# Kernel tuning notes

Hardware: AMD Instinct MI355X
Metric: run time of the kernel (lower is better)

The kernel has to match this reference:

```python
import jax, jax.numpy as jnp
import numpy as np

N_NODES = 50000
N_EDGES = 600000
NODE_DIM = 64
EDGE_DIM = 16
HIDDEN = 128
N_LAYERS = 3
N_CLASSES = 2
N_GRAPHS = 256
BN_EPS = 1e-5


def setup_inputs() -> dict:
    key = jax.random.key(0)
    ks = jax.random.split(key, 24)
    i = iter(range(24))
    def nrm(shape, scale=0.05):
        return jax.random.normal(ks[next(i)], shape, dtype=jnp.float32) * scale
    inp = {
        "x": jax.random.normal(ks[next(i)], (N_NODES, NODE_DIM), dtype=jnp.float32),
        "edge_index": jax.random.randint(ks[next(i)], (2, N_EDGES), 0, N_NODES),
        "edge_attr": jax.random.normal(ks[next(i)], (N_EDGES, EDGE_DIM), dtype=jnp.float32),
        "batch": jnp.sort(jax.random.randint(ks[next(i)], (N_NODES,), 0, N_GRAPHS)),
        # encoders
        "node_w": nrm((NODE_DIM, HIDDEN)), "node_b": jnp.zeros((HIDDEN,), jnp.float32),
        "edge_w": nrm((EDGE_DIM, HIDDEN)), "edge_b": jnp.zeros((HIDDEN,), jnp.float32),
        # per-layer GINE MLP params, stacked over layers
        "mlp_w1": nrm((N_LAYERS, HIDDEN, HIDDEN)), "mlp_b1": jnp.zeros((N_LAYERS, HIDDEN), jnp.float32),
        "mlp_w2": nrm((N_LAYERS, HIDDEN, HIDDEN)), "mlp_b2": jnp.zeros((N_LAYERS, HIDDEN), jnp.float32),
        "bn_gamma": jnp.ones((N_LAYERS, HIDDEN), jnp.float32), "bn_beta": jnp.zeros((N_LAYERS, HIDDEN), jnp.float32),
        # head
        "head_w1": nrm((HIDDEN, HIDDEN)), "head_b1": jnp.zeros((HIDDEN,), jnp.float32),
        "head_w2": nrm((HIDDEN, N_CLASSES)), "head_b2": jnp.zeros((N_CLASSES,), jnp.float32),
    }
    return inp


def _forward(x, edge_attr, node_w, node_b, edge_w, edge_b, mlp_w1, mlp_b1,
             mlp_w2, mlp_b2, bn_gamma, bn_beta, head_w1, head_b1, head_w2,
             head_b2, edge_index, batch):
    src, dst = edge_index[0], edge_index[1]
    h = x @ node_w + node_b                     # [N, H]
    ea = edge_attr @ edge_w + edge_b            # [E, H]
    for l in range(N_LAYERS):
        # GINE message: relu(x_src + edge_attr), scatter-add into dst
        msg = jax.nn.relu(h[src] + ea)          # [E, H]
        agg = jax.ops.segment_sum(msg, dst, num_segments=N_NODES)
        z = h + agg                              # (1+eps)*x + agg, eps=0
        z = jax.nn.relu(z @ mlp_w1[l] + mlp_b1[l]) @ mlp_w2[l] + mlp_b2[l]
        # BatchNorm1d over node dim (batch statistics)
        mean = jnp.mean(z, axis=0)
        var = jnp.var(z, axis=0)
        z = bn_gamma[l] * (z - mean) * jax.lax.rsqrt(var + BN_EPS) + bn_beta[l]
        h = jax.nn.relu(z)                       # dropout off (eval)
    g = jax.ops.segment_sum(h, batch, num_segments=N_GRAPHS)  # global_add_pool
    return jax.nn.relu(g @ head_w1 + head_b1) @ head_w2 + head_b2


def reference(x, edge_index, edge_attr, batch, node_w, node_b, edge_w, edge_b,
              mlp_w1, mlp_b1, mlp_w2, mlp_b2, bn_gamma, bn_beta,
              head_w1, head_b1, head_w2, head_b2):
    return _forward(x, edge_attr, node_w, node_b, edge_w, edge_b, mlp_w1,
                    mlp_b1, mlp_w2, mlp_b2, bn_gamma, bn_beta, head_w1,
                    head_b1, head_w2, head_b2, edge_index, batch)
```

## Files before the change

### kernel.cpp

```cpp
#include <hip/hip_runtime.h>

#define N_NODES_C 50000
#define N_EDGES_C 600000
#define NODE_DIM_C 64
#define EDGE_DIM_C 16
#define HID 128
#define N_GRAPHS_C 256
#define BN_EPS_C 1e-5f
#define SCAN_NBLK ((N_NODES_C + 255) / 256)

typedef short bf16x8 __attribute__((ext_vector_type(8)));
typedef float f32x4 __attribute__((ext_vector_type(4)));
typedef float f32x2 __attribute__((ext_vector_type(2)));

__device__ __forceinline__ unsigned short f2bf(float f) {
  union { float f; unsigned u; } v; v.f = f;
  unsigned r = (v.u + 0x7fffu + ((v.u >> 16) & 1u)) >> 16;
  return (unsigned short)r;
}

__device__ __forceinline__ float2 bfp2f(unsigned u) {
  union { unsigned u; float f; } lo, hi;
  lo.u = u << 16;
  hi.u = u & 0xffff0000u;
  return make_float2(lo.f, hi.f);
}

__device__ __forceinline__ float bf2f(unsigned short s) {
  union { unsigned u; float f; } v;
  v.u = ((unsigned)s) << 16;
  return v.f;
}

__device__ __forceinline__ float2 fp8p2f(unsigned short u) {
  f32x2 r = __builtin_amdgcn_cvt_pk_f32_fp8((int)(unsigned)u, false);
  return make_float2(r.x, r.y);
}

__global__ __launch_bounds__(256)
void k_x2bf(const float* __restrict__ x, unsigned short* __restrict__ xb,
            int* __restrict__ cnt, float* __restrict__ g) {
  int tid = blockIdx.x * 256 + threadIdx.x;
  size_t i = (size_t)tid * 4;
  if (i < (size_t)N_NODES_C * NODE_DIM_C) {
    float4 v = *(const float4*)&x[i];
    uint2 o;
    o.x = (unsigned)f2bf(v.x) | ((unsigned)f2bf(v.y) << 16);
    o.y = (unsigned)f2bf(v.z) | ((unsigned)f2bf(v.w) << 16);
    *(uint2*)&xb[i] = o;
  }
  if (tid < N_NODES_C) cnt[tid] = 0;
  if (tid < N_GRAPHS_C * HID) g[tid] = 0.f;
}

__global__ __launch_bounds__(256)
void k_prep_w(const float* __restrict__ w1, const float* __restrict__ w2,
              const float* __restrict__ nodew, unsigned short* __restrict__ wT) {
  int m = blockIdx.x;
  if (m < 6) {
    const float* src = (m < 3) ? (w1 + (size_t)m * HID * HID)
                               : (w2 + (size_t)(m - 3) * HID * HID);
    unsigned short* dst = wT + (size_t)m * HID * HID;
    for (int i = threadIdx.x; i < HID * HID; i += 256) {
      int n = i >> 7, k = i & 127;
      dst[n * HID + k] = f2bf(src[k * HID + n]);
    }
  } else {
    unsigned short* dst = wT + (size_t)6 * HID * HID;
    for (int i = threadIdx.x; i < HID * NODE_DIM_C; i += 256) {
      int n = i >> 6, k = i & 63;
      dst[n * NODE_DIM_C + k] = f2bf(nodew[k * HID + n]);
    }
  }
}

__global__ __launch_bounds__(256)
void k_node_mfma(const unsigned short* __restrict__ xb,
                 const unsigned short* __restrict__ nwT,
                 const float* __restrict__ bias, unsigned short* __restrict__ h) {
  const int LD = NODE_DIM_C + 8;
  __shared__ unsigned short a_lds[128 * LD];
  __shared__ unsigned short w_lds[128 * LD];
  int t = threadIdx.x;
  int row0 = blockIdx.x * 128;
  {
    int r = t >> 3, c = t & 7;
#pragma unroll
    for (int it = 0; it < 4; ++it) {
      int row = it * 32 + r;
      int grow = row0 + row;
      uint4 va = (grow < N_NODES_C)
                     ? ((const uint4*)(xb + (size_t)grow * NODE_DIM_C))[c]
                     : make_uint4(0, 0, 0, 0);
      *(uint4*)&a_lds[row * LD + c * 8] = va;
      uint4 vw = ((const uint4*)(nwT + (size_t)row * NODE_DIM_C))[c];
      *(uint4*)&w_lds[row * LD + c * 8] = vw;
    }
  }
  __syncthreads();

  int lane = t & 63;
  int w = t >> 6;
  int l15 = lane & 15;
  int q = lane >> 4;

  f32x4 acc[2][8];
#pragma unroll
  for (int rt = 0; rt < 2; ++rt)
#pragma unroll
    for (int nt = 0; nt < 8; ++nt) acc[rt][nt] = (f32x4)0.f;

#pragma unroll
  for (int kk = 0; kk < 2; ++kk) {
    int k0 = kk * 32;
    bf16x8 af[2];
#pragma unroll
    for (int rt = 0; rt < 2; ++rt) {
      int arow = w * 32 + rt * 16 + l15;
      af[rt] = *(const bf16x8*)&a_lds[arow * LD + k0 + q * 8];
    }
#pragma unroll
    for (int nt = 0; nt < 8; ++nt) {
      bf16x8 bf = *(const bf16x8*)&w_lds[(nt * 16 + l15) * LD + k0 + q * 8];
#pragma unroll
      for (int rt = 0; rt < 2; ++rt)
        acc[rt][nt] = __builtin_amdgcn_mfma_f32_16x16x32_bf16(af[rt], bf, acc[rt][nt], 0, 0, 0);
    }
  }

#pragma unroll
  for (int nt = 0; nt < 8; ++nt) {
    int gcol = nt * 16 + l15;
    float bv = bias[gcol];
#pragma unroll
    for (int rt = 0; rt < 2; ++rt) {
#pragma unroll
      for (int i = 0; i < 4; ++i) {
        int grow = row0 + w * 32 + rt * 16 + q * 4 + i;
        if (grow < N_NODES_C) h[(size_t)grow * HID + gcol] = f2bf(acc[rt][nt][i] + bv);
      }
    }
  }
}

__global__ __launch_bounds__(256)
void k_histogram(const int* __restrict__ dst, int* __restrict__ counts) {
  int e = blockIdx.x * 256 + threadIdx.x;
  if (e < N_EDGES_C) atomicAdd(&counts[dst[e]], 1);
}

__global__ __launch_bounds__(256)
void k_blocksum(const int* __restrict__ cnt, int* __restrict__ partial) {
  __shared__ int ls[4];
  int t = threadIdx.x;
  int i = blockIdx.x * 256 + t;
  int v = (i < N_NODES_C) ? cnt[i] : 0;
#pragma unroll
  for (int o = 32; o > 0; o >>= 1) v += __shfl_down(v, o, 64);
  if ((t & 63) == 0) ls[t >> 6] = v;
  __syncthreads();
  if (t == 0) partial[blockIdx.x] = ls[0] + ls[1] + ls[2] + ls[3];
}

__global__ __launch_bounds__(256)
void k_scanpartials(const int* __restrict__ partial, int* __restrict__ partial_off) {
  __shared__ int s[256];
  int t = threadIdx.x;
  int v = (t < SCAN_NBLK) ? partial[t] : 0;
  s[t] = v;
  __syncthreads();
  for (int d = 1; d < 256; d <<= 1) {
    int x = (t >= d) ? s[t - d] : 0;
    __syncthreads();
    s[t] += x;
    __syncthreads();
  }
  if (t < SCAN_NBLK) partial_off[t] = s[t] - v;
}

__global__ __launch_bounds__(256)
void k_apply(int* __restrict__ cnt_cursor, const int* __restrict__ partial_off,
             int* __restrict__ row_ptr) {
  __shared__ int s[256];
  int t = threadIdx.x;
  int i = blockIdx.x * 256 + t;
  int v = (i < N_NODES_C) ? cnt_cursor[i] : 0;
  s[t] = v;
  __syncthreads();
  for (int d = 1; d < 256; d <<= 1) {
    int x = (t >= d) ? s[t - d] : 0;
    __syncthreads();
    s[t] += x;
    __syncthreads();
  }
  int excl = s[t] - v + partial_off[blockIdx.x];
  if (i < N_NODES_C) {
    row_ptr[i] = excl;
    cnt_cursor[i] = excl;
  }
  if (i == 0) row_ptr[N_NODES_C] = N_EDGES_C;
}

__global__ __launch_bounds__(256)
void k_bucket(const int* __restrict__ dst, const int* __restrict__ srcArr,
              int* __restrict__ cursor, int* __restrict__ perm,
              int* __restrict__ src_perm) {
  int e = blockIdx.x * 256 + threadIdx.x;
  if (e < N_EDGES_C) {
    int p = atomicAdd(&cursor[dst[e]], 1);
    perm[p] = e;
    src_perm[p] = srcArr[e];
  }
}

#define EE_LDW 40
#define EE_OSW 132
__global__ __launch_bounds__(256)
void k_edge_encode(const int* __restrict__ perm, const float* __restrict__ eattr,
                   const float* __restrict__ ew, const float* __restrict__ ebias,
                   unsigned char* __restrict__ ea8) {
  __shared__ unsigned short smem[128 * EE_OSW];
  unsigned short* a_lds = smem;
  unsigned short* w_lds = smem + 128 * EE_LDW;
  int t = threadIdx.x;
  int EB = blockIdx.x * 128;

  if (t < 128) {
    unsigned short tmp[16];
#pragma unroll
    for (int k = 0; k < 16; ++k) tmp[k] = f2bf(ew[k * HID + t]);
    uint4* wr = (uint4*)&w_lds[t * EE_LDW];
    wr[0] = *(uint4*)&tmp[0];
    wr[1] = *(uint4*)&tmp[8];
    wr[2] = make_uint4(0, 0, 0, 0);
    wr[3] = make_uint4(0, 0, 0, 0);
  }
  {
    int edge = t >> 1, half = t & 1;
    int gi = EB + edge;
    float4 v0 = make_float4(0, 0, 0, 0), v1 = v0;
    if (gi < N_EDGES_C) {
      int e = perm[gi];
      const float4* p = (const float4*)(eattr + (size_t)e * EDGE_DIM_C + half * 8);
      v0 = p[0];
      v1 = p[1];
    }
    unsigned short tmp[8] = {f2bf(v0.x), f2bf(v0.y), f2bf(v0.z), f2bf(v0.w),
                             f2bf(v1.x), f2bf(v1.y), f2bf(v1.z), f2bf(v1.w)};
    *(uint4*)&a_lds[edge * EE_LDW + half * 8] = *(uint4*)tmp;
    *(uint4*)&a_lds[edge * EE_LDW + 16 + half * 8] = make_uint4(0, 0, 0, 0);
  }
  __syncthreads();

  int lane = t & 63;
  int w = t >> 6;
  int l15 = lane & 15;
  int q = lane >> 4;

  f32x4 acc[2][8];
  {
    bf16x8 af[2];
#pragma unroll
    for (int rt = 0; rt < 2; ++rt) {
      int arow = w * 32 + rt * 16 + l15;
      af[rt] = *(const bf16x8*)&a_lds[arow * EE_LDW + q * 8];
    }
#pragma unroll
    for (int nt = 0; nt < 8; ++nt) {
      bf16x8 bf = *(const bf16x8*)&w_lds[(nt * 16 + l15) * EE_LDW + q * 8];
#pragma unroll
      for (int rt = 0; rt < 2; ++rt)
        acc[rt][nt] = __builtin_amdgcn_mfma_f32_16x16x32_bf16(
            af[rt], bf, (f32x4)0.f, 0, 0, 0);
    }
  }
  __syncthreads();

#pragma unroll
  for (int nt = 0; nt < 8; ++nt) {
    int col = nt * 16 + l15;
    float bv = ebias[col];
#pragma unroll
    for (int rt = 0; rt < 2; ++rt) {
#pragma unroll
      for (int i = 0; i < 4; ++i) {
        int row = w * 32 + rt * 16 + q * 4 + i;
        smem[row * EE_OSW + col] = f2bf(acc[rt][nt][i] + bv);
      }
    }
  }
  __syncthreads();

  int valid = min(128, N_EDGES_C - EB);
  for (int i = t; i < valid * 32; i += 256) {
    int row = i >> 5, c = i & 31;
    uint2 v = *(const uint2*)&smem[row * EE_OSW + c * 4];
    float2 p0 = bfp2f(v.x);
    float2 p1 = bfp2f(v.y);
    int r = __builtin_amdgcn_cvt_pk_fp8_f32(p0.x, p0.y, 0, false);
    r = __builtin_amdgcn_cvt_pk_fp8_f32(p1.x, p1.y, r, true);
    *(unsigned*)&ea8[((size_t)EB + row) * 128 + c * 4] = (unsigned)r;
  }
}

__global__ __launch_bounds__(256)
void k_aggregate(const unsigned* __restrict__ h32, const unsigned char* __restrict__ ea8,
                 const int* __restrict__ src_p, const int* __restrict__ row_ptr,
                 unsigned short* __restrict__ z, float* __restrict__ gsum,
                 float* __restrict__ gsumsq) {
  int t = threadIdx.x;
  if (blockIdx.x == 0 && t < HID) { gsum[t] = 0.f; gsumsq[t] = 0.f; }
  int lane = t & 63;
  int wave = t >> 6;
  int node = blockIdx.x * 4 + wave;
  if (node >= N_NODES_C) return;
  float2 base = bfp2f(h32[(size_t)node * 64 + lane]);
  float acc0 = base.x, acc1 = base.y;
  int beg = row_ptr[node], end = row_ptr[node + 1];
  const unsigned char* eap = ea8 + lane * 2;
  int j = beg;
  for (; j + 8 <= end; j += 8) {
    int s0 = src_p[j],     s1 = src_p[j + 1], s2 = src_p[j + 2], s3 = src_p[j + 3];
    int s4 = src_p[j + 4], s5 = src_p[j + 5], s6 = src_p[j + 6], s7 = src_p[j + 7];
    unsigned g0 = h32[(size_t)s0 * 64 + lane];
    unsigned g1 = h32[(size_t)s1 * 64 + lane];
    unsigned g2 = h32[(size_t)s2 * 64 + lane];
    unsigned g3 = h32[(size_t)s3 * 64 + lane];
    unsigned g4 = h32[(size_t)s4 * 64 + lane];
    unsigned g5 = h32[(size_t)s5 * 64 + lane];
    unsigned g6 = h32[(size_t)s6 * 64 + lane];
    unsigned g7 = h32[(size_t)s7 * 64 + lane];
    unsigned short u0 = *(const unsigned short*)(eap + (size_t)j * 128);
    unsigned short u1 = *(const unsigned short*)(eap + (size_t)(j + 1) * 128);
    unsigned short u2 = *(const unsigned short*)(eap + (size_t)(j + 2) * 128);
    unsigned short u3 = *(const unsigned short*)(eap + (size_t)(j + 3) * 128);
    unsigned short u4 = *(const unsigned short*)(eap + (size_t)(j + 4) * 128);
    unsigned short u5 = *(const unsigned short*)(eap + (size_t)(j + 5) * 128);
    unsigned short u6 = *(const unsigned short*)(eap + (size_t)(j + 6) * 128);
    unsigned short u7 = *(const unsigned short*)(eap + (size_t)(j + 7) * 128);
    float2 a0 = bfp2f(g0), a1 = bfp2f(g1), a2 = bfp2f(g2), a3 = bfp2f(g3);
    float2 a4 = bfp2f(g4), a5 = bfp2f(g5), a6 = bfp2f(g6), a7 = bfp2f(g7);
    float2 e0 = fp8p2f(u0), e1 = fp8p2f(u1), e2 = fp8p2f(u2), e3 = fp8p2f(u3);
    float2 e4 = fp8p2f(u4), e5 = fp8p2f(u5), e6 = fp8p2f(u6), e7 = fp8p2f(u7);
    acc0 += fmaxf(a0.x + e0.x, 0.f) + fmaxf(a1.x + e1.x, 0.f) +
            fmaxf(a2.x + e2.x, 0.f) + fmaxf(a3.x + e3.x, 0.f) +
            fmaxf(a4.x + e4.x, 0.f) + fmaxf(a5.x + e5.x, 0.f) +
            fmaxf(a6.x + e6.x, 0.f) + fmaxf(a7.x + e7.x, 0.f);
    acc1 += fmaxf(a0.y + e0.y, 0.f) + fmaxf(a1.y + e1.y, 0.f) +
            fmaxf(a2.y + e2.y, 0.f) + fmaxf(a3.y + e3.y, 0.f) +
            fmaxf(a4.y + e4.y, 0.f) + fmaxf(a5.y + e5.y, 0.f) +
            fmaxf(a6.y + e6.y, 0.f) + fmaxf(a7.y + e7.y, 0.f);
  }
  for (; j + 4 <= end; j += 4) {
    int s0 = src_p[j], s1 = src_p[j + 1], s2 = src_p[j + 2], s3 = src_p[j + 3];
    unsigned g0 = h32[(size_t)s0 * 64 + lane];
    unsigned g1 = h32[(size_t)s1 * 64 + lane];
    unsigned g2 = h32[(size_t)s2 * 64 + lane];
    unsigned g3 = h32[(size_t)s3 * 64 + lane];
    unsigned short u0 = *(const unsigned short*)(eap + (size_t)j * 128);
    unsigned short u1 = *(const unsigned short*)(eap + (size_t)(j + 1) * 128);
    unsigned short u2 = *(const unsigned short*)(eap + (size_t)(j + 2) * 128);
    unsigned short u3 = *(const unsigned short*)(eap + (size_t)(j + 3) * 128);
    float2 a0 = bfp2f(g0), a1 = bfp2f(g1), a2 = bfp2f(g2), a3 = bfp2f(g3);
    float2 e0 = fp8p2f(u0), e1 = fp8p2f(u1), e2 = fp8p2f(u2), e3 = fp8p2f(u3);
    acc0 += fmaxf(a0.x + e0.x, 0.f) + fmaxf(a1.x + e1.x, 0.f) +
            fmaxf(a2.x + e2.x, 0.f) + fmaxf(a3.x + e3.x, 0.f);
    acc1 += fmaxf(a0.y + e0.y, 0.f) + fmaxf(a1.y + e1.y, 0.f) +
            fmaxf(a2.y + e2.y, 0.f) + fmaxf(a3.y + e3.y, 0.f);
  }
  for (; j < end; ++j) {
    int s0 = src_p[j];
    float2 a0 = bfp2f(h32[(size_t)s0 * 64 + lane]);
    float2 e0 = fp8p2f(*(const unsigned short*)(eap + (size_t)j * 128));
    acc0 += fmaxf(a0.x + e0.x, 0.f);
    acc1 += fmaxf(a0.y + e0.y, 0.f);
  }
  unsigned packed = (unsigned)f2bf(acc0) | ((unsigned)f2bf(acc1) << 16);
  *(unsigned*)&z[(size_t)node * HID + lane * 2] = packed;
}

template <bool RELU, bool STATS>
__global__ __launch_bounds__(256)
void k_gemm_mfma(const unsigned short* __restrict__ in,
                 const unsigned short* __restrict__ wT,
                 const float* __restrict__ bias,
                 unsigned short* __restrict__ outb,
                 float* __restrict__ gsum, float* __restrict__ gsumsq) {
  const int LDA = HID + 8;
  __shared__ unsigned short a_lds[128 * LDA];
  __shared__ unsigned short w_lds[128 * LDA];
  int t = threadIdx.x;
  int row0 = blockIdx.x * 128;
  {
    int r = t >> 4, chunk = t & 15;
#pragma unroll
    for (int it = 0; it < 8; ++it) {
      int row = it * 16 + r;
      int grow = row0 + row;
      uint4 va = (grow < N_NODES_C)
                     ? ((const uint4*)(in + (size_t)grow * HID))[chunk]
                     : make_uint4(0, 0, 0, 0);
      *(uint4*)&a_lds[row * LDA + chunk * 8] = va;
      uint4 vw = ((const uint4*)(wT + (size_t)row * HID))[chunk];
      *(uint4*)&w_lds[row * LDA + chunk * 8] = vw;
    }
  }
  __syncthreads();

  int lane = t & 63;
  int w = t >> 6;
  int l15 = lane & 15;
  int q = lane >> 4;

  f32x4 acc[2][8];
#pragma unroll
  for (int rt = 0; rt < 2; ++rt)
#pragma unroll
    for (int nt = 0; nt < 8; ++nt) acc[rt][nt] = (f32x4)0.f;

#pragma unroll
  for (int kk = 0; kk < 4; ++kk) {
    int k0 = kk * 32;
    bf16x8 af[2];
#pragma unroll
    for (int rt = 0; rt < 2; ++rt) {
      int arow = w * 32 + rt * 16 + l15;
      af[rt] = *(const bf16x8*)&a_lds[arow * LDA + k0 + q * 8];
    }
#pragma unroll
    for (int nt = 0; nt < 8; ++nt) {
      int brow = nt * 16 + l15;
      bf16x8 bf = *(const bf16x8*)&w_lds[brow * LDA + k0 + q * 8];
#pragma unroll
      for (int rt = 0; rt < 2; ++rt)
        acc[rt][nt] = __builtin_amdgcn_mfma_f32_16x16x32_bf16(af[rt], bf, acc[rt][nt], 0, 0, 0);
    }
  }

  float sp[8], qp[8];
#pragma unroll
  for (int nt = 0; nt < 8; ++nt) { sp[nt] = 0.f; qp[nt] = 0.f; }

#pragma unroll
  for (int nt = 0; nt < 8; ++nt) {
    int gcol = nt * 16 + l15;
    float bv = bias[gcol];
#pragma unroll
    for (int rt = 0; rt < 2; ++rt) {
#pragma unroll
      for (int i = 0; i < 4; ++i) {
        int grow = row0 + w * 32 + rt * 16 + q * 4 + i;
        bool ok = (grow < N_NODES_C);
        float v = acc[rt][nt][i] + bv;
        if (RELU) v = fmaxf(v, 0.f);
        if (ok) outb[(size_t)grow * HID + gcol] = f2bf(v);
        if (STATS) {
          float c = ok ? v : 0.f;
          sp[nt] += c;
          qp[nt] += c * c;
        }
      }
    }
  }

  if (STATS) {
    __syncthreads();
    float* sred = (float*)a_lds;
    float* qred = sred + 128 * 16;
    int slot = w * 4 + q;
#pragma unroll
    for (int nt = 0; nt < 8; ++nt) {
      int gcol = nt * 16 + l15;
      sred[gcol * 16 + slot] = sp[nt];
      qred[gcol * 16 + slot] = qp[nt];
    }
    __syncthreads();
    if (t < 128) {
      float s = 0.f;
#pragma unroll
      for (int i = 0; i < 16; ++i) s += sred[t * 16 + i];
      atomicAdd(&gsum[t], s);
    } else {
      int f = t - 128;
      float s = 0.f;
#pragma unroll
      for (int i = 0; i < 16; ++i) s += qred[f * 16 + i];
      atomicAdd(&gsumsq[f], s);
    }
  }
}

__global__ __launch_bounds__(256)
void k_bn_relu(const unsigned short* __restrict__ t2, const float* __restrict__ gsum,
               const float* __restrict__ gsumsq, const float* __restrict__ gamma,
               const float* __restrict__ beta, unsigned short* __restrict__ h) {
  __shared__ float sc[HID], sh[HID];
  int t = threadIdx.x;
  if (t < HID) {
    float mean = gsum[t] * (1.f / N_NODES_C);
    float var = gsumsq[t] * (1.f / N_NODES_C) - mean * mean;
    float inv = rsqrtf(var + BN_EPS_C);
    float s = gamma[t] * inv;
    sc[t] = s;
    sh[t] = beta[t] - mean * s;
  }
  __syncthreads();
  size_t idx = ((size_t)blockIdx.x * 256 + t) * 8;
  if (idx < (size_t)N_NODES_C * HID) {
    uint4 v = *(const uint4*)&t2[idx];
    int f = (int)(idx & 127);
    float2 p0 = bfp2f(v.x), p1 = bfp2f(v.y), p2 = bfp2f(v.z), p3 = bfp2f(v.w);
    float r0 = fmaxf(p0.x * sc[f + 0] + sh[f + 0], 0.f);
    float r1 = fmaxf(p0.y * sc[f + 1] + sh[f + 1], 0.f);
    float r2 = fmaxf(p1.x * sc[f + 2] + sh[f + 2], 0.f);
    float r3 = fmaxf(p1.y * sc[f + 3] + sh[f + 3], 0.f);
    float r4 = fmaxf(p2.x * sc[f + 4] + sh[f + 4], 0.f);
    float r5 = fmaxf(p2.y * sc[f + 5] + sh[f + 5], 0.f);
    float r6 = fmaxf(p3.x * sc[f + 6] + sh[f + 6], 0.f);
    float r7 = fmaxf(p3.y * sc[f + 7] + sh[f + 7], 0.f);
    uint4 o;
    o.x = (unsigned)f2bf(r0) | ((unsigned)f2bf(r1) << 16);
    o.y = (unsigned)f2bf(r2) | ((unsigned)f2bf(r3) << 16);
    o.z = (unsigned)f2bf(r4) | ((unsigned)f2bf(r5) << 16);
    o.w = (unsigned)f2bf(r6) | ((unsigned)f2bf(r7) << 16);
    *(uint4*)&h[idx] = o;
  }
}

__global__ __launch_bounds__(128)
void k_bn_relu_pool(const unsigned short* __restrict__ t2, const float* __restrict__ gsum,
                    const float* __restrict__ gsumsq, const float* __restrict__ gamma,
                    const float* __restrict__ beta, const int* __restrict__ batch,
                    float* __restrict__ g) {
  int t = threadIdx.x;
  float mean = gsum[t] * (1.f / N_NODES_C);
  float var = gsumsq[t] * (1.f / N_NODES_C) - mean * mean;
  float inv = rsqrtf(var + BN_EPS_C);
  float sc = gamma[t] * inv;
  float sh = beta[t] - mean * sc;
  int n0 = blockIdx.x * 64;
  if (n0 >= N_NODES_C) return;
  int end = min(n0 + 64, N_NODES_C);
  int cur = batch[n0];
  float acc = 0.f;
  for (int n = n0; n < end; ++n) {
    int b = batch[n];
    if (b != cur) {
      atomicAdd(&g[cur * HID + t], acc);
      acc = 0.f;
      cur = b;
    }
    acc += fmaxf(bf2f(t2[(size_t)n * HID + t]) * sc + sh, 0.f);
  }
  atomicAdd(&g[cur * HID + t], acc);
}

__global__ __launch_bounds__(128)
void k_head(const float* __restrict__ g, const float* __restrict__ w1,
            const float* __restrict__ b1, const float* __restrict__ w2,
            const float* __restrict__ b2, float* __restrict__ out) {
  __shared__ float gs[HID];
  __shared__ float red[HID * 2];
  int gi = blockIdx.x, t = threadIdx.x;
  gs[t] = g[gi * HID + t];
  __syncthreads();
  float acc = b1[t];
#pragma unroll 8
  for (int k = 0; k < HID; ++k) acc += gs[k] * w1[k * HID + t];
  float hid = fmaxf(acc, 0.f);
  red[t * 2] = hid * w2[t * 2];
  red[t * 2 + 1] = hid * w2[t * 2 + 1];
  __syncthreads();
  for (int s = 64; s > 0; s >>= 1) {
    if (t < s) { red[t * 2] += red[(t + s) * 2]; red[t * 2 + 1] += red[(t + s) * 2 + 1]; }
    __syncthreads();
  }
  if (t == 0) {
    out[gi * 2] = red[0] + b2[0];
    out[gi * 2 + 1] = red[1] + b2[1];
  }
}

extern "C" void kernel_launch(void* const* d_in, const int* in_sizes, int n_in,
                              void* d_out, int out_size, void* d_ws, size_t ws_size,
                              hipStream_t stream) {
  const float* x      = (const float*)d_in[0];
  const int*   eidx   = (const int*)d_in[1];
  const float* eattr  = (const float*)d_in[2];
  const int*   batch  = (const int*)d_in[3];
  const float* node_w = (const float*)d_in[4];
  const float* node_b = (const float*)d_in[5];
  const float* edge_w = (const float*)d_in[6];
  const float* edge_b = (const float*)d_in[7];
  const float* mlp_w1 = (const float*)d_in[8];
  const float* mlp_b1 = (const float*)d_in[9];
  const float* mlp_w2 = (const float*)d_in[10];
  const float* mlp_b2 = (const float*)d_in[11];
  const float* bn_g   = (const float*)d_in[12];
  const float* bn_b   = (const float*)d_in[13];
  const float* hw1    = (const float*)d_in[14];
  const float* hb1    = (const float*)d_in[15];
  const float* hw2    = (const float*)d_in[16];
  const float* hb2    = (const float*)d_in[17];
  const int* srcArr = eidx;
  const int* dstArr = eidx + N_EDGES_C;

  char* wsp = (char*)d_ws;
  size_t off = 0;
  auto alloc = [&](size_t bytes) {
    void* p = wsp + off;
    off += (bytes + 255) & ~(size_t)255;
    return p;
  };
  unsigned short* h    = (unsigned short*)alloc((size_t)N_NODES_C * HID * 2);
  unsigned short* zbf  = (unsigned short*)alloc((size_t)N_NODES_C * HID * 2);
  unsigned short* t1bf = (unsigned short*)alloc((size_t)N_NODES_C * HID * 2);
  unsigned short* t2bf = (unsigned short*)alloc((size_t)N_NODES_C * HID * 2);
  unsigned char* ea8   = (unsigned char*)alloc((size_t)N_EDGES_C * HID);
  unsigned short* xb   = (unsigned short*)alloc((size_t)N_NODES_C * NODE_DIM_C * 2);
  unsigned short* wT   = (unsigned short*)alloc(((size_t)6 * HID * HID + HID * NODE_DIM_C) * 2);
  int* row_ptr   = (int*)alloc((N_NODES_C + 1) * 4);
  int* cnt_cur   = (int*)alloc(N_NODES_C * 4);
  int* perm      = (int*)alloc((size_t)N_EDGES_C * 4);
  int* src_perm  = (int*)alloc((size_t)N_EDGES_C * 4);
  int* partial   = (int*)alloc(256 * 4);
  int* partial_off = (int*)alloc(256 * 4);
  float* gsum    = (float*)alloc(HID * 4);
  float* gsumsq  = (float*)alloc(HID * 4);
  float* g       = (float*)alloc((size_t)N_GRAPHS_C * HID * 4);
  unsigned short* nwT = wT + (size_t)6 * HID * HID;

  k_x2bf<<<(N_NODES_C * NODE_DIM_C / 4 + 255) / 256, 256, 0, stream>>>(x, xb,
                                                                       cnt_cur, g);
  k_prep_w<<<7, 256, 0, stream>>>(mlp_w1, mlp_w2, node_w, wT);
  k_node_mfma<<<(N_NODES_C + 127) / 128, 256, 0, stream>>>(xb, nwT, node_b, h);
  k_histogram<<<(N_EDGES_C + 255) / 256, 256, 0, stream>>>(dstArr, cnt_cur);
  k_blocksum<<<SCAN_NBLK, 256, 0, stream>>>(cnt_cur, partial);
  k_scanpartials<<<1, 256, 0, stream>>>(partial, partial_off);
  k_apply<<<SCAN_NBLK, 256, 0, stream>>>(cnt_cur, partial_off, row_ptr);
  k_bucket<<<(N_EDGES_C + 255) / 256, 256, 0, stream>>>(dstArr, srcArr, cnt_cur,
                                                        perm, src_perm);
  k_edge_encode<<<(N_EDGES_C + 127) / 128, 256, 0, stream>>>(perm, eattr, edge_w,
                                                             edge_b, ea8);

  const int GB = (N_NODES_C + 127) / 128;
  for (int l = 0; l < 3; ++l) {
    k_aggregate<<<(N_NODES_C + 3) / 4, 256, 0, stream>>>((const unsigned*)h, ea8,
                                                         src_perm, row_ptr, zbf,
                                                         gsum, gsumsq);
    k_gemm_mfma<true, false><<<GB, 256, 0, stream>>>(
        zbf, wT + (size_t)l * HID * HID, mlp_b1 + l * HID, t1bf, nullptr, nullptr);
    k_gemm_mfma<false, true><<<GB, 256, 0, stream>>>(
        t1bf, wT + (size_t)(3 + l) * HID * HID, mlp_b2 + l * HID, t2bf,
        gsum, gsumsq);
    if (l < 2) {
      k_bn_relu<<<(N_NODES_C * HID / 8 + 255) / 256, 256, 0, stream>>>(
          t2bf, gsum, gsumsq, bn_g + l * HID, bn_b + l * HID, h);
    } else {
      k_bn_relu_pool<<<(N_NODES_C + 63) / 64, 128, 0, stream>>>(
          t2bf, gsum, gsumsq, bn_g + l * HID, bn_b + l * HID, batch, g);
    }
  }
  k_head<<<N_GRAPHS_C, 128, 0, stream>>>(g, hw1, hb1, hw2, hb2, (float*)d_out);
}
```

Before: 517.1 us.

## Fuse two MLP GEMMs into one kernel and pack bucket edge data

Merges the two per-layer MLP GEMM kernels into one. The ReLU'd hidden tile stays in LDS as bf16 and the second weight matrix is loaded into the freed weight buffer, so the t1 intermediate no longer makes a global round trip and three launches per forward are removed. Separately, the bucket kernel now writes (edge id, src) as a single int2 scatter, and the edge encoder writes the permuted src array with coalesced stores. This trades a little extra LDS traffic and serialization inside the fused kernel for less global memory traffic.

```diff
diff --git a/kernel.cpp b/kernel.cpp
--- a/kernel.cpp
+++ b/kernel.cpp
@@ -203,22 +203,22 @@
 
 __global__ __launch_bounds__(256)
 void k_bucket(const int* __restrict__ dst, const int* __restrict__ srcArr,
-              int* __restrict__ cursor, int* __restrict__ perm,
-              int* __restrict__ src_perm) {
+              int* __restrict__ cursor, int2* __restrict__ edata) {
   int e = blockIdx.x * 256 + threadIdx.x;
   if (e < N_EDGES_C) {
-    int p = atomicAdd(&cursor[dst[e]], 1);
-    perm[p] = e;
-    src_perm[p] = srcArr[e];
+    int d = dst[e];
+    int s = srcArr[e];
+    int p = atomicAdd(&cursor[d], 1);
+    edata[p] = make_int2(e, s);
   }
 }
 
 #define EE_LDW 40
 #define EE_OSW 132
 __global__ __launch_bounds__(256)
-void k_edge_encode(const int* __restrict__ perm, const float* __restrict__ eattr,
+void k_edge_encode(const int2* __restrict__ edata, const float* __restrict__ eattr,
                    const float* __restrict__ ew, const float* __restrict__ ebias,
-                   unsigned char* __restrict__ ea8) {
+                   unsigned char* __restrict__ ea8, int* __restrict__ src_perm) {
   __shared__ unsigned short smem[128 * EE_OSW];
   unsigned short* a_lds = smem;
   unsigned short* w_lds = smem + 128 * EE_LDW;
@@ -240,8 +240,9 @@
     int gi = EB + edge;
     float4 v0 = make_float4(0, 0, 0, 0), v1 = v0;
     if (gi < N_EDGES_C) {
-      int e = perm[gi];
-      const float4* p = (const float4*)(eattr + (size_t)e * EDGE_DIM_C + half * 8);
+      int2 ed = edata[gi];
+      if (half == 0) src_perm[gi] = ed.y;
+      const float4* p = (const float4*)(eattr + (size_t)ed.x * EDGE_DIM_C + half * 8);
       v0 = p[0];
       v1 = p[1];
     }
@@ -379,14 +380,16 @@
   *(unsigned*)&z[(size_t)node * HID + lane * 2] = packed;
 }
 
-template <bool RELU, bool STATS>
-__global__ __launch_bounds__(256)
-void k_gemm_mfma(const unsigned short* __restrict__ in,
-                 const unsigned short* __restrict__ wT,
-                 const float* __restrict__ bias,
+__global__ __launch_bounds__(256)
+void k_mlp_fused(const unsigned short* __restrict__ in,
+                 const unsigned short* __restrict__ w1T,
+                 const float* __restrict__ b1,
+                 const unsigned short* __restrict__ w2T,
+                 const float* __restrict__ b2,
                  unsigned short* __restrict__ outb,
                  float* __restrict__ gsum, float* __restrict__ gsumsq) {
   const int LDA = HID + 8;
+  const int OS = 132;
   __shared__ unsigned short a_lds[128 * LDA];
   __shared__ unsigned short w_lds[128 * LDA];
   int t = threadIdx.x;
@@ -401,7 +404,7 @@
                      ? ((const uint4*)(in + (size_t)grow * HID))[chunk]
                      : make_uint4(0, 0, 0, 0);
       *(uint4*)&a_lds[row * LDA + chunk * 8] = va;
-      uint4 vw = ((const uint4*)(wT + (size_t)row * HID))[chunk];
+      uint4 vw = ((const uint4*)(w1T + (size_t)row * HID))[chunk];
       *(uint4*)&w_lds[row * LDA + chunk * 8] = vw;
     }
   }
@@ -436,6 +439,55 @@
         acc[rt][nt] = __builtin_amdgcn_mfma_f32_16x16x32_bf16(af[rt], bf, acc[rt][nt], 0, 0, 0);
     }
   }
+  __syncthreads();
+
+#pragma unroll
+  for (int nt = 0; nt < 8; ++nt) {
+    int col = nt * 16 + l15;
+    float bv = b1[col];
+#pragma unroll
+    for (int rt = 0; rt < 2; ++rt) {
+#pragma unroll
+      for (int i = 0; i < 4; ++i) {
+        int row = w * 32 + rt * 16 + q * 4 + i;
+        a_lds[row * OS + col] = f2bf(fmaxf(acc[rt][nt][i] + bv, 0.f));
+      }
+    }
+  }
+  {
+    int r = t >> 4, chunk = t & 15;
+#pragma unroll
+    for (int it = 0; it < 8; ++it) {
+      int row = it * 16 + r;
+      uint4 vw = ((const uint4*)(w2T + (size_t)row * HID))[chunk];
+      *(uint4*)&w_lds[row * LDA + chunk * 8] = vw;
+    }
+  }
+  __syncthreads();
+
+#pragma unroll
+  for (int rt = 0; rt < 2; ++rt)
+#pragma unroll
+    for (int nt = 0; nt < 8; ++nt) acc[rt][nt] = (f32x4)0.f;
+
+#pragma unroll
+  for (int kk = 0; kk < 4; ++kk) {
+    int k0 = kk * 32;
+    bf16x8 af[2];
+#pragma unroll
+    for (int rt = 0; rt < 2; ++rt) {
+      int arow = w * 32 + rt * 16 + l15;
+      af[rt] = *(const bf16x8*)&a_lds[arow * OS + k0 + q * 8];
+    }
+#pragma unroll
+    for (int nt = 0; nt < 8; ++nt) {
+      int brow = nt * 16 + l15;
+      bf16x8 bf = *(const bf16x8*)&w_lds[brow * LDA + k0 + q * 8];
+#pragma unroll
+      for (int rt = 0; rt < 2; ++rt)
+        acc[rt][nt] = __builtin_amdgcn_mfma_f32_16x16x32_bf16(af[rt], bf, acc[rt][nt], 0, 0, 0);
+    }
+  }
 
   float sp[8], qp[8];
 #pragma unroll
@@ -444,7 +496,7 @@
 #pragma unroll
   for (int nt = 0; nt < 8; ++nt) {
     int gcol = nt * 16 + l15;
-    float bv = bias[gcol];
+    float bv = b2[gcol];
 #pragma unroll
     for (int rt = 0; rt < 2; ++rt) {
 #pragma unroll
@@ -452,41 +504,36 @@
         int grow = row0 + w * 32 + rt * 16 + q * 4 + i;
         bool ok = (grow < N_NODES_C);
         float v = acc[rt][nt][i] + bv;
-        if (RELU) v = fmaxf(v, 0.f);
         if (ok) outb[(size_t)grow * HID + gcol] = f2bf(v);
-        if (STATS) {
-          float c = ok ? v : 0.f;
-          sp[nt] += c;
-          qp[nt] += c * c;
-        }
+        float c = ok ? v : 0.f;
+        sp[nt] += c;
+        qp[nt] += c * c;
       }
     }
   }
 
-  if (STATS) {
-    __syncthreads();
-    float* sred = (float*)a_lds;
-    float* qred = sred + 128 * 16;
-    int slot = w * 4 + q;
-#pragma unroll
-    for (int nt = 0; nt < 8; ++nt) {
-      int gcol = nt * 16 + l15;
-      sred[gcol * 16 + slot] = sp[nt];
-      qred[gcol * 16 + slot] = qp[nt];
-    }
-    __syncthreads();
-    if (t < 128) {
-      float s = 0.f;
-#pragma unroll
-      for (int i = 0; i < 16; ++i) s += sred[t * 16 + i];
-      atomicAdd(&gsum[t], s);
-    } else {
-      int f = t - 128;
-      float s = 0.f;
-#pragma unroll
-      for (int i = 0; i < 16; ++i) s += qred[f * 16 + i];
-      atomicAdd(&gsumsq[f], s);
-    }
+  __syncthreads();
+  float* sred = (float*)a_lds;
+  float* qred = sred + 128 * 16;
+  int slot = w * 4 + q;
+#pragma unroll
+  for (int nt = 0; nt < 8; ++nt) {
+    int gcol = nt * 16 + l15;
+    sred[gcol * 16 + slot] = sp[nt];
+    qred[gcol * 16 + slot] = qp[nt];
+  }
+  __syncthreads();
+  if (t < 128) {
+    float s = 0.f;
+#pragma unroll
+    for (int i = 0; i < 16; ++i) s += sred[t * 16 + i];
+    atomicAdd(&gsum[t], s);
+  } else {
+    int f = t - 128;
+    float s = 0.f;
+#pragma unroll
+    for (int i = 0; i < 16; ++i) s += qred[f * 16 + i];
+    atomicAdd(&gsumsq[f], s);
   }
 }
 
@@ -614,14 +661,13 @@
   };
   unsigned short* h    = (unsigned short*)alloc((size_t)N_NODES_C * HID * 2);
   unsigned short* zbf  = (unsigned short*)alloc((size_t)N_NODES_C * HID * 2);
-  unsigned short* t1bf = (unsigned short*)alloc((size_t)N_NODES_C * HID * 2);
   unsigned short* t2bf = (unsigned short*)alloc((size_t)N_NODES_C * HID * 2);
   unsigned char* ea8   = (unsigned char*)alloc((size_t)N_EDGES_C * HID);
   unsigned short* xb   = (unsigned short*)alloc((size_t)N_NODES_C * NODE_DIM_C * 2);
   unsigned short* wT   = (unsigned short*)alloc(((size_t)6 * HID * HID + HID * NODE_DIM_C) * 2);
   int* row_ptr   = (int*)alloc((N_NODES_C + 1) * 4);
   int* cnt_cur   = (int*)alloc(N_NODES_C * 4);
-  int* perm      = (int*)alloc((size_t)N_EDGES_C * 4);
+  int2* edata    = (int2*)alloc((size_t)N_EDGES_C * 8);
   int* src_perm  = (int*)alloc((size_t)N_EDGES_C * 4);
   int* partial   = (int*)alloc(256 * 4);
   int* partial_off = (int*)alloc(256 * 4);
@@ -639,20 +685,18 @@
   k_scanpartials<<<1, 256, 0, stream>>>(partial, partial_off);
   k_apply<<<SCAN_NBLK, 256, 0, stream>>>(cnt_cur, partial_off, row_ptr);
   k_bucket<<<(N_EDGES_C + 255) / 256, 256, 0, stream>>>(dstArr, srcArr, cnt_cur,
-                                                        perm, src_perm);
-  k_edge_encode<<<(N_EDGES_C + 127) / 128, 256, 0, stream>>>(perm, eattr, edge_w,
-                                                             edge_b, ea8);
+                                                        edata);
+  k_edge_encode<<<(N_EDGES_C + 127) / 128, 256, 0, stream>>>(edata, eattr, edge_w,
+                                                             edge_b, ea8, src_perm);
 
   const int GB = (N_NODES_C + 127) / 128;
   for (int l = 0; l < 3; ++l) {
     k_aggregate<<<(N_NODES_C + 3) / 4, 256, 0, stream>>>((const unsigned*)h, ea8,
                                                          src_perm, row_ptr, zbf,
                                                          gsum, gsumsq);
-    k_gemm_mfma<true, false><<<GB, 256, 0, stream>>>(
-        zbf, wT + (size_t)l * HID * HID, mlp_b1 + l * HID, t1bf, nullptr, nullptr);
-    k_gemm_mfma<false, true><<<GB, 256, 0, stream>>>(
-        t1bf, wT + (size_t)(3 + l) * HID * HID, mlp_b2 + l * HID, t2bf,
-        gsum, gsumsq);
+    k_mlp_fused<<<GB, 256, 0, stream>>>(
+        zbf, wT + (size_t)l * HID * HID, mlp_b1 + l * HID,
+        wT + (size_t)(3 + l) * HID * HID, mlp_b2 + l * HID, t2bf, gsum, gsumsq);
     if (l < 2) {
       k_bn_relu<<<(N_NODES_C * HID / 8 + 255) / 256, 256, 0, stream>>>(
           t2bf, gsum, gsumsq, bn_g + l * HID, bn_b + l * HID, h);
```

Result: faster. 479.6 us (-7.3%).
